# Kernel optimization log

Measured on AMD Instinct MI355X. Metric: run time of the kernel, lower is better.

Reference implementation:

```python
import jax, jax.numpy as jnp
import numpy as np

N, E, F, H, D, O = 100000, 1600000, 128, 128, 64, 1


def setup_inputs() -> dict:
    key = jax.random.key(0)
    ks = jax.random.split(key, 10)
    s = lambda f: np.float32(1.0 / np.sqrt(f))
    return {
        "x": jax.random.normal(ks[0], (N, F), jnp.float32),
        "edge_index": jax.random.randint(ks[1], (2, E), 0, N),
        "W1": jax.random.normal(ks[2], (F, H), jnp.float32) * s(F),
        "b1": jnp.zeros((H,), jnp.float32),
        "Wh": jax.random.normal(ks[3], (H, H), jnp.float32) * s(H),
        "bh": jnp.zeros((H,), jnp.float32),
        "W2": jax.random.normal(ks[4], (H, D), jnp.float32) * s(H),
        "b2": jnp.zeros((D,), jnp.float32),
        "Wo": jax.random.normal(ks[5], (D, O), jnp.float32) * s(D),
        "bo": jnp.zeros((O,), jnp.float32),
    }


def _gcn_layer(h, W, b, src, dst, norm, n):
    # linear transform then normalized sparse aggregation (GCNConv)
    h = h @ W                                   # [n, out]
    msg = h[src] * norm[:, None]                # gather + scale, [E+n, out]
    return jax.ops.segment_sum(msg, dst, num_segments=n) + b


def reference(x, edge_index, W1, b1, Wh, bh, W2, b2, Wo, bo):
    n = x.shape[0]
    loop = jnp.arange(n, dtype=edge_index.dtype)
    src = jnp.concatenate([edge_index[0], loop])  # add self loops
    dst = jnp.concatenate([edge_index[1], loop])
    deg = jax.ops.segment_sum(jnp.ones_like(dst, dtype=x.dtype), dst, num_segments=n)
    dinv = jnp.where(deg > 0, jax.lax.rsqrt(deg), 0.0)
    norm = dinv[src] * dinv[dst]                  # sym-normalized edge weights

    h = jax.nn.relu(_gcn_layer(x, W1, b1, src, dst, norm, n))
    h = jax.nn.relu(_gcn_layer(h, Wh, bh, src, dst, norm, n))
    z = _gcn_layer(h, W2, b2, src, dst, norm, n)  # embedding (no relu after gcn2)
    return z @ Wo + bo                            # node_classification logits [n, 1]
```

## Files before the change

kernel.cpp:

```cpp
#include <hip/hip_runtime.h>
#include <hip/hip_fp16.h>


#define CHUNK 8192
#define ASTR 136

using f16x8 = __attribute__((ext_vector_type(8))) _Float16;
using f32x4 = __attribute__((ext_vector_type(4))) float;

__global__ __launch_bounds__(256) void prep_w(const float* __restrict__ W1,
                                              const float* __restrict__ Wh,
                                              const float* __restrict__ W2,
                                              const float* __restrict__ b2,
                                              const float* __restrict__ Wo,
                                              const float* __restrict__ bo,
                                              __half* __restrict__ Wt1,
                                              __half* __restrict__ WtH,
                                              float* __restrict__ w3,
                                              float* __restrict__ c3) {
    const float* W = blockIdx.x ? Wh : W1;
    __half* Wt = blockIdx.x ? WtH : Wt1;
    for (int i = threadIdx.x; i < 16384; i += 256) {
        int c = i >> 7, k = i & 127;
        Wt[c * 128 + k] = __float2half(W[k * 128 + c]);
    }
    if (blockIdx.x == 0 && threadIdx.x < 128) {
        int j = threadIdx.x;
        float s = 0.f;
        for (int d = 0; d < 64; ++d) s += W2[j * 64 + d] * Wo[d];
        w3[j] = s;
        if (j == 0) {
            float c = 0.f;
            for (int d = 0; d < 64; ++d) c += b2[d] * Wo[d];
            *c3 = c + bo[0];
        }
    }
}

__device__ __forceinline__ void hist_body(const int* __restrict__ dst,
                                          int* __restrict__ hist,
                                          int E, int NBKT, int NB, int blk) {
    __shared__ int bins[1024];
    for (int i = threadIdx.x; i < NBKT; i += 256) bins[i] = 0;
    __syncthreads();
    int beg = blk * CHUNK, end = min(E, beg + CHUNK);
    for (int e = beg + threadIdx.x; e < end; e += 256)
        atomicAdd(&bins[dst[e] >> 7], 1);
    __syncthreads();
    for (int i = threadIdx.x; i < NBKT; i += 256)
        hist[i * NB + blk] = bins[i];
}

template<typename AT>
__device__ __forceinline__ void gemm_body(const AT* __restrict__ A,
                                          const __half* __restrict__ Wt,
                                          __half* __restrict__ Ch, int n, int blk) {
    __shared__ _Float16 Al[64 * ASTR];
    __shared__ _Float16 Wl[128 * ASTR];
    const int tid = threadIdx.x;
    const int row0 = blk * 64;

#pragma unroll
    for (int i = 0; i < 8; ++i) {
        int idx = tid + 256 * i;
        int c = idx >> 4, q = idx & 15;
        uint4 v = *(const uint4*)(Wt + c * 128 + q * 8);
        *(uint4*)(&Wl[c * ASTR + q * 8]) = v;
    }
#pragma unroll
    for (int i = 0; i < 4; ++i) {
        int idx = tid + 256 * i;
        int r = idx >> 4, q = idx & 15;
        int row = row0 + r;
        uint4 u;
        if constexpr (sizeof(AT) == 2) {
            u = (row < n) ? *(const uint4*)((const __half*)A + (size_t)row * 128 + q * 8)
                          : make_uint4(0u, 0u, 0u, 0u);
        } else {
            if (row < n) {
                const float* ap = (const float*)A + (size_t)row * 128 + q * 8;
                float4 v0 = *(const float4*)ap;
                float4 v1 = *(const float4*)(ap + 4);
                __half2 p0 = __floats2half2_rn(v0.x, v0.y);
                __half2 p1 = __floats2half2_rn(v0.z, v0.w);
                __half2 p2 = __floats2half2_rn(v1.x, v1.y);
                __half2 p3 = __floats2half2_rn(v1.z, v1.w);
                u.x = *(unsigned*)&p0; u.y = *(unsigned*)&p1;
                u.z = *(unsigned*)&p2; u.w = *(unsigned*)&p3;
            } else u = make_uint4(0u, 0u, 0u, 0u);
        }
        *(uint4*)(&Al[r * ASTR + q * 8]) = u;
    }
    __syncthreads();

    const int wave = tid >> 6, lane = tid & 63;
    const int wr = (wave >> 1) * 32;
    const int wc = (wave & 1) * 64;
    const int l = lane & 15, g = lane >> 4;

    f32x4 acc[2][4];
#pragma unroll
    for (int i = 0; i < 2; ++i)
#pragma unroll
        for (int j = 0; j < 4; ++j) acc[i][j] = (f32x4){0.f, 0.f, 0.f, 0.f};

#pragma unroll
    for (int kk = 0; kk < 128; kk += 32) {
        int ko = kk + g * 8;
        f16x8 a0 = *(const f16x8*)(&Al[(wr + l) * ASTR + ko]);
        f16x8 a1 = *(const f16x8*)(&Al[(wr + 16 + l) * ASTR + ko]);
        f16x8 b0 = *(const f16x8*)(&Wl[(wc + l) * ASTR + ko]);
        f16x8 b1 = *(const f16x8*)(&Wl[(wc + 16 + l) * ASTR + ko]);
        f16x8 b2 = *(const f16x8*)(&Wl[(wc + 32 + l) * ASTR + ko]);
        f16x8 b3 = *(const f16x8*)(&Wl[(wc + 48 + l) * ASTR + ko]);
        acc[0][0] = __builtin_amdgcn_mfma_f32_16x16x32_f16(a0, b0, acc[0][0], 0, 0, 0);
        acc[0][1] = __builtin_amdgcn_mfma_f32_16x16x32_f16(a0, b1, acc[0][1], 0, 0, 0);
        acc[0][2] = __builtin_amdgcn_mfma_f32_16x16x32_f16(a0, b2, acc[0][2], 0, 0, 0);
        acc[0][3] = __builtin_amdgcn_mfma_f32_16x16x32_f16(a0, b3, acc[0][3], 0, 0, 0);
        acc[1][0] = __builtin_amdgcn_mfma_f32_16x16x32_f16(a1, b0, acc[1][0], 0, 0, 0);
        acc[1][1] = __builtin_amdgcn_mfma_f32_16x16x32_f16(a1, b1, acc[1][1], 0, 0, 0);
        acc[1][2] = __builtin_amdgcn_mfma_f32_16x16x32_f16(a1, b2, acc[1][2], 0, 0, 0);
        acc[1][3] = __builtin_amdgcn_mfma_f32_16x16x32_f16(a1, b3, acc[1][3], 0, 0, 0);
    }

#pragma unroll
    for (int rt = 0; rt < 2; ++rt) {
#pragma unroll
        for (int j = 0; j < 4; ++j) {
            int row = row0 + wr + rt * 16 + g * 4 + j;
            if (row < n) {
#pragma unroll
                for (int ct = 0; ct < 4; ++ct)
                    Ch[(size_t)row * 128 + wc + ct * 16 + l] =
                        __float2half(acc[rt][ct][j]);
            }
        }
    }
}

__global__ __launch_bounds__(256) void mega1(const int* __restrict__ dst,
                                             int* __restrict__ hist,
                                             int E, int NBKT, int NB,
                                             const float* __restrict__ x,
                                             const __half* __restrict__ Wt1,
                                             __half* __restrict__ g1, int n) {
    if ((int)blockIdx.x < NB)
        hist_body(dst, hist, E, NBKT, NB, blockIdx.x);
    else
        gemm_body<float>(x, Wt1, g1, n, blockIdx.x - NB);
}

__global__ __launch_bounds__(256) void gemm2_k(const __half* __restrict__ A,
                                               const __half* __restrict__ Wt,
                                               __half* __restrict__ Ch, int n) {
    gemm_body<__half>(A, Wt, Ch, n, blockIdx.x);
}

__global__ __launch_bounds__(256) void scanA(int* __restrict__ hist, int* __restrict__ binsum,
                                             int NBKT, int NB) {
    int wave = (int)((blockIdx.x * (size_t)blockDim.x + threadIdx.x) >> 6);
    if (wave >= NBKT) return;
    int lane = threadIdx.x & 63;
    int* row = hist + (size_t)wave * NB;
    int running = 0;
    for (int b0 = 0; b0 < NB; b0 += 64) {
        int idx = b0 + lane;
        int v = (idx < NB) ? row[idx] : 0;
        int s = v;
#pragma unroll
        for (int off = 1; off < 64; off <<= 1) {
            int u = __shfl_up(s, off, 64);
            if (lane >= off) s += u;
        }
        if (idx < NB) row[idx] = running + s - v;
        running += __shfl(s, 63, 64);
    }
    if (lane == 0) binsum[wave] = running;
}

__global__ void scanK2(const int* __restrict__ binsum, int* __restrict__ binbase,
                       int NBKT, int E) {
    __shared__ int s[1024];
    int t = threadIdx.x;
    int v = (t < NBKT) ? binsum[t] : 0;
    s[t] = v;
    __syncthreads();
    for (int off = 1; off < 1024; off <<= 1) {
        int u = (t >= off) ? s[t - off] : 0;
        __syncthreads();
        s[t] += u;
        __syncthreads();
    }
    if (t < NBKT) binbase[t] = s[t] - v;
    if (t == 0) binbase[NBKT] = E;
}

__global__ __launch_bounds__(256) void scatterH(const int* __restrict__ src,
                                                const int* __restrict__ dst,
                                                const int* __restrict__ hist,
                                                const int* __restrict__ binbase,
                                                int* __restrict__ tmp,
                                                int E, int NBKT, int NB) {
    __shared__ int offs[1024];
    int blk = blockIdx.x;
    for (int i = threadIdx.x; i < NBKT; i += 256)
        offs[i] = hist[i * NB + blk] + binbase[i];
    __syncthreads();
    int beg = blk * CHUNK, end = min(E, beg + CHUNK);
    for (int e = beg + threadIdx.x; e < end; e += 256) {
        int d = dst[e];
        int pos = atomicAdd(&offs[d >> 7], 1);
        tmp[pos] = ((d & 127) << 17) | src[e];
    }
}

#define EBUF 2688
__global__ __launch_bounds__(256) void bucket_csr(const int* __restrict__ tmp,
                                                  const int* __restrict__ binbase,
                                                  int* __restrict__ rowptr,
                                                  int* __restrict__ srcidx,
                                                  float* __restrict__ dinv,
                                                  int n) {
    __shared__ int cnt[128], sc[128], cnt2[128];
    __shared__ int ebuf[EBUF];
    int b = blockIdx.x;
    int bstart = binbase[b], bend = binbase[b + 1];
    int cntE = bend - bstart;
    bool fit = (cntE <= EBUF);
    if (threadIdx.x < 128) cnt[threadIdx.x] = 0;
    __syncthreads();
    for (int e = threadIdx.x; e < cntE; e += 256) {
        int p = tmp[bstart + e];
        if (fit) ebuf[e] = p;
        atomicAdd(&cnt[p >> 17], 1);
    }
    __syncthreads();
    if (threadIdx.x < 128) sc[threadIdx.x] = cnt[threadIdx.x];
    __syncthreads();
    for (int off = 1; off < 128; off <<= 1) {
        int u = 0;
        if (threadIdx.x < 128 && threadIdx.x >= off) u = sc[threadIdx.x - off];
        __syncthreads();
        if (threadIdx.x < 128) sc[threadIdx.x] += u;
        __syncthreads();
    }
    if (threadIdx.x < 128) {
        int excl = sc[threadIdx.x] - cnt[threadIdx.x];
        cnt2[threadIdx.x] = excl;
        int id = b * 128 + threadIdx.x;
        if (id <= n) rowptr[id] = bstart + excl;
        if (id < n) dinv[id] = rsqrtf((float)cnt[threadIdx.x] + 1.0f);
    }
    __syncthreads();
    for (int e = threadIdx.x; e < cntE; e += 256) {
        int p = fit ? ebuf[e] : tmp[bstart + e];
        int pos = bstart + atomicAdd(&cnt2[p >> 17], 1);
        srcidx[pos] = p & 0x1FFFF;
    }
}

template<int MODE, int EDGE_DINV>
__global__ __launch_bounds__(256) void agg_csr(const int* __restrict__ rowptr,
                                               const int* __restrict__ srcidx,
                                               const float* __restrict__ dinv,
                                               const __half* __restrict__ Gh,
                                               const float* __restrict__ bias,
                                               const float* __restrict__ w3,
                                               void* __restrict__ outp, int n) {
    int node = (int)((blockIdx.x * (size_t)blockDim.x + threadIdx.x) >> 5);
    if (node >= n) return;
    const int lane = threadIdx.x & 63;
    const int l32 = lane & 31;
    const int strm = l32 >> 4;
    const int l = l32 & 15;
    const int co = l * 8;
    int beg = rowptr[node], end = rowptr[node + 1];
    float di = dinv[node];

    float4 aLo = make_float4(0.f, 0.f, 0.f, 0.f);
    float4 aHi = make_float4(0.f, 0.f, 0.f, 0.f);

#define ACCS(u, s)                                                          \
    {                                                                       \
        float2 f0 = __half22float2(*(const __half2*)&(u).x);                \
        float2 f1 = __half22float2(*(const __half2*)&(u).y);                \
        float2 f2 = __half22float2(*(const __half2*)&(u).z);                \
        float2 f3 = __half22float2(*(const __half2*)&(u).w);                \
        aLo.x = fmaf(f0.x, s, aLo.x); aLo.y = fmaf(f0.y, s, aLo.y);         \
        aLo.z = fmaf(f1.x, s, aLo.z); aLo.w = fmaf(f1.y, s, aLo.w);         \
        aHi.x = fmaf(f2.x, s, aHi.x); aHi.y = fmaf(f2.y, s, aHi.y);         \
        aHi.z = fmaf(f3.x, s, aHi.z); aHi.w = fmaf(f3.y, s, aHi.w);         \
    }

    if (strm == 0) {
        uint4 u = *(const uint4*)(Gh + (size_t)node * 128 + co);
        float sf = EDGE_DINV ? di : 1.0f;
        ACCS(u, sf);
    }

    int e = beg + strm;
    for (; e + 6 < end; e += 8) {
        int s0 = srcidx[e], s1 = srcidx[e + 2], s2 = srcidx[e + 4], s3 = srcidx[e + 6];
        float d0 = 1.f, d1 = 1.f, d2 = 1.f, d3 = 1.f;
        if (EDGE_DINV) { d0 = dinv[s0]; d1 = dinv[s1]; d2 = dinv[s2]; d3 = dinv[s3]; }
        uint4 u0 = *(const uint4*)(Gh + (size_t)s0 * 128 + co);
        uint4 u1 = *(const uint4*)(Gh + (size_t)s1 * 128 + co);
        uint4 u2 = *(const uint4*)(Gh + (size_t)s2 * 128 + co);
        uint4 u3 = *(const uint4*)(Gh + (size_t)s3 * 128 + co);
        ACCS(u0, d0);
        ACCS(u1, d1);
        ACCS(u2, d2);
        ACCS(u3, d3);
    }
    for (; e < end; e += 2) {
        int s0 = srcidx[e];
        float d0 = EDGE_DINV ? dinv[s0] : 1.0f;
        uint4 u0 = *(const uint4*)(Gh + (size_t)s0 * 128 + co);
        ACCS(u0, d0);
    }
#undef ACCS

    aLo.x += __shfl_xor(aLo.x, 16, 64); aLo.y += __shfl_xor(aLo.y, 16, 64);
    aLo.z += __shfl_xor(aLo.z, 16, 64); aLo.w += __shfl_xor(aLo.w, 16, 64);
    aHi.x += __shfl_xor(aHi.x, 16, 64); aHi.y += __shfl_xor(aHi.y, 16, 64);
    aHi.z += __shfl_xor(aHi.z, 16, 64); aHi.w += __shfl_xor(aHi.w, 16, 64);

    float4 b0 = *(const float4*)(bias + co);
    float4 b1 = *(const float4*)(bias + co + 4);
    float o0 = fmaxf(di * aLo.x + b0.x, 0.f);
    float o1 = fmaxf(di * aLo.y + b0.y, 0.f);
    float o2 = fmaxf(di * aLo.z + b0.z, 0.f);
    float o3 = fmaxf(di * aLo.w + b0.w, 0.f);
    float o4 = fmaxf(di * aHi.x + b1.x, 0.f);
    float o5 = fmaxf(di * aHi.y + b1.y, 0.f);
    float o6 = fmaxf(di * aHi.z + b1.z, 0.f);
    float o7 = fmaxf(di * aHi.w + b1.w, 0.f);

    if constexpr (MODE == 0) {
        if (strm == 0) {
            __half2 p0 = __floats2half2_rn(di * o0, di * o1);
            __half2 p1 = __floats2half2_rn(di * o2, di * o3);
            __half2 p2 = __floats2half2_rn(di * o4, di * o5);
            __half2 p3 = __floats2half2_rn(di * o6, di * o7);
            uint4 u;
            u.x = *(unsigned*)&p0; u.y = *(unsigned*)&p1;
            u.z = *(unsigned*)&p2; u.w = *(unsigned*)&p3;
            *(uint4*)((__half*)outp + (size_t)node * 128 + co) = u;
        }
    } else {
        float4 w0 = *(const float4*)(w3 + co);
        float4 w1 = *(const float4*)(w3 + co + 4);
        float v = o0 * w0.x + o1 * w0.y + o2 * w0.z + o3 * w0.w
                + o4 * w1.x + o5 * w1.y + o6 * w1.z + o7 * w1.w;
        v += __shfl_xor(v, 1, 64);
        v += __shfl_xor(v, 2, 64);
        v += __shfl_xor(v, 4, 64);
        v += __shfl_xor(v, 8, 64);
        if (l32 == 0) ((float*)outp)[node] = di * v;
    }
}

__global__ void agg_csr_scalar(const int* __restrict__ rowptr, const int* __restrict__ srcidx,
                               const float* __restrict__ dinv, const float* __restrict__ ys,
                               const float* __restrict__ c3, float* __restrict__ out, int n) {
    int i = blockIdx.x * blockDim.x + threadIdx.x;
    if (i >= n) return;
    int beg = rowptr[i], end = rowptr[i + 1];
    float acc = ys[i];
    int e = beg;
    for (; e + 3 < end; e += 4) {
        acc += ys[srcidx[e]] + ys[srcidx[e + 1]] + ys[srcidx[e + 2]] + ys[srcidx[e + 3]];
    }
    for (; e < end; ++e) acc += ys[srcidx[e]];
    out[i] = dinv[i] * acc + c3[0];
}

static inline size_t align4(size_t x) { return (x + 3) & ~(size_t)3; }

extern "C" void kernel_launch(void* const* d_in, const int* in_sizes, int n_in,
                              void* d_out, int out_size, void* d_ws, size_t ws_size,
                              hipStream_t stream) {
    const float* x  = (const float*)d_in[0];
    const int* ei   = (const int*)d_in[1];
    const float* W1 = (const float*)d_in[2];
    const float* b1 = (const float*)d_in[3];
    const float* Wh = (const float*)d_in[4];
    const float* bh = (const float*)d_in[5];
    const float* W2 = (const float*)d_in[6];
    const float* b2 = (const float*)d_in[7];
    const float* Wo = (const float*)d_in[8];
    const float* bo = (const float*)d_in[9];
    float* out = (float*)d_out;

    const int n = in_sizes[0] / 128;
    const int E = in_sizes[1] / 2;
    const int* src = ei;
    const int* dst = ei + E;

    const int NB = (E + CHUNK - 1) / CHUNK;
    const int NBKT = (n >> 7) + 1;

    size_t o = 0;
    int* rowptr = (int*)d_ws + o;        o = align4(o + n + 1);
    int* srcidx = (int*)d_ws + o;        o = align4(o + E);
    int* tmp    = (int*)d_ws + o;        o = align4(o + E);
    int* hist   = (int*)d_ws + o;        o = align4(o + (size_t)NBKT * NB);
    int* binsum = (int*)d_ws + o;        o = align4(o + NBKT);
    int* binbase= (int*)d_ws + o;        o = align4(o + NBKT + 1);
    float* dinv = (float*)d_ws + o;      o = align4(o + n);
    float* w3   = (float*)d_ws + o;      o = align4(o + 128);
    float* c3   = (float*)d_ws + o;      o = align4(o + 4);
    __half* Wt1 = (__half*)((int*)d_ws + o);     o = align4(o + 8192);
    __half* WtH = (__half*)((int*)d_ws + o);     o = align4(o + 8192);
    __half* bufA16 = (__half*)((int*)d_ws + o);  o = align4(o + (size_t)n * 64);
    __half* bufB16 = (__half*)((int*)d_ws + o);  o = align4(o + (size_t)n * 64);
    float* ys = (float*)bufB16;

    const int B = (n + 255) / 256;
    const int GG = (n + 63) / 64;
    const int GA = (int)(((size_t)n * 32 + 255) / 256);

    prep_w<<<2, 256, 0, stream>>>(W1, Wh, W2, b2, Wo, bo, Wt1, WtH, w3, c3);

    mega1<<<NB + GG, 256, 0, stream>>>(dst, hist, E, NBKT, NB, x, Wt1, bufA16, n);

    scanA<<<(NBKT * 64 + 255) / 256, 256, 0, stream>>>(hist, binsum, NBKT, NB);
    scanK2<<<1, 1024, 0, stream>>>(binsum, binbase, NBKT, E);
    scatterH<<<NB, 256, 0, stream>>>(src, dst, hist, binbase, tmp, E, NBKT, NB);
    bucket_csr<<<NBKT, 256, 0, stream>>>(tmp, binbase, rowptr, srcidx, dinv, n);

    agg_csr<0, 1><<<GA, 256, 0, stream>>>(rowptr, srcidx, dinv, bufA16, b1, w3, bufB16, n);

    gemm2_k<<<GG, 256, 0, stream>>>(bufB16, WtH, bufA16, n);
    agg_csr<1, 0><<<GA, 256, 0, stream>>>(rowptr, srcidx, dinv, bufA16, bh, w3, ys, n);

    agg_csr_scalar<<<B, 256, 0, stream>>>(rowptr, srcidx, dinv, ys, c3, out, n);
}
```

Baseline: 222.4 us.

## Regroup kernel launches: fuse weight prep with histogram, scatter with first GEMM

Weight transpose and conversion now runs as two extra blocks of the histogram kernel, removing the separate prep_w launch. The first-layer GEMM moves out of that kernel into a combined launch with the edge scatter, so the GEMM runs concurrently with scattering instead of with histogramming. The intent is to save one launch and let the scatter work overlap the GEMM. As a side effect the histogram kernel runs alone, with only two small prep blocks alongside it.

```diff
diff --git a/kernel.cpp b/kernel.cpp
--- a/kernel.cpp
+++ b/kernel.cpp
@@ -8,23 +8,38 @@
 using f16x8 = __attribute__((ext_vector_type(8))) _Float16;
 using f32x4 = __attribute__((ext_vector_type(4))) float;
 
-__global__ __launch_bounds__(256) void prep_w(const float* __restrict__ W1,
-                                              const float* __restrict__ Wh,
-                                              const float* __restrict__ W2,
-                                              const float* __restrict__ b2,
-                                              const float* __restrict__ Wo,
-                                              const float* __restrict__ bo,
-                                              __half* __restrict__ Wt1,
-                                              __half* __restrict__ WtH,
-                                              float* __restrict__ w3,
-                                              float* __restrict__ c3) {
-    const float* W = blockIdx.x ? Wh : W1;
-    __half* Wt = blockIdx.x ? WtH : Wt1;
+__device__ __forceinline__ void hist_body(const int* __restrict__ dst,
+                                          int* __restrict__ hist,
+                                          int E, int NBKT, int NB, int blk) {
+    __shared__ int bins[1024];
+    for (int i = threadIdx.x; i < NBKT; i += 256) bins[i] = 0;
+    __syncthreads();
+    int beg = blk * CHUNK, end = min(E, beg + CHUNK);
+    for (int e = beg + threadIdx.x; e < end; e += 256)
+        atomicAdd(&bins[dst[e] >> 7], 1);
+    __syncthreads();
+    for (int i = threadIdx.x; i < NBKT; i += 256)
+        hist[i * NB + blk] = bins[i];
+}
+
+__device__ __forceinline__ void prep_body(int which,
+                                          const float* __restrict__ W1,
+                                          const float* __restrict__ Wh,
+                                          const float* __restrict__ W2,
+                                          const float* __restrict__ b2,
+                                          const float* __restrict__ Wo,
+                                          const float* __restrict__ bo,
+                                          __half* __restrict__ Wt1,
+                                          __half* __restrict__ WtH,
+                                          float* __restrict__ w3,
+                                          float* __restrict__ c3) {
+    const float* W = which ? Wh : W1;
+    __half* Wt = which ? WtH : Wt1;
     for (int i = threadIdx.x; i < 16384; i += 256) {
         int c = i >> 7, k = i & 127;
         Wt[c * 128 + k] = __float2half(W[k * 128 + c]);
     }
-    if (blockIdx.x == 0 && threadIdx.x < 128) {
+    if (which == 0 && threadIdx.x < 128) {
         int j = threadIdx.x;
         float s = 0.f;
         for (int d = 0; d < 64; ++d) s += W2[j * 64 + d] * Wo[d];
@@ -37,18 +52,22 @@
     }
 }
 
-__device__ __forceinline__ void hist_body(const int* __restrict__ dst,
-                                          int* __restrict__ hist,
-                                          int E, int NBKT, int NB, int blk) {
-    __shared__ int bins[1024];
-    for (int i = threadIdx.x; i < NBKT; i += 256) bins[i] = 0;
+__device__ __forceinline__ void scatter_body(const int* __restrict__ src,
+                                             const int* __restrict__ dst,
+                                             const int* __restrict__ hist,
+                                             const int* __restrict__ binbase,
+                                             int* __restrict__ tmp,
+                                             int E, int NBKT, int NB, int blk) {
+    __shared__ int offs[1024];
+    for (int i = threadIdx.x; i < NBKT; i += 256)
+        offs[i] = hist[i * NB + blk] + binbase[i];
     __syncthreads();
     int beg = blk * CHUNK, end = min(E, beg + CHUNK);
-    for (int e = beg + threadIdx.x; e < end; e += 256)
-        atomicAdd(&bins[dst[e] >> 7], 1);
-    __syncthreads();
-    for (int i = threadIdx.x; i < NBKT; i += 256)
-        hist[i * NB + blk] = bins[i];
+    for (int e = beg + threadIdx.x; e < end; e += 256) {
+        int d = dst[e];
+        int pos = atomicAdd(&offs[d >> 7], 1);
+        tmp[pos] = ((d & 127) << 17) | src[e];
+    }
 }
 
 template<typename AT>
@@ -141,11 +160,33 @@
 __global__ __launch_bounds__(256) void mega1(const int* __restrict__ dst,
                                              int* __restrict__ hist,
                                              int E, int NBKT, int NB,
+                                             const float* __restrict__ W1,
+                                             const float* __restrict__ Wh,
+                                             const float* __restrict__ W2,
+                                             const float* __restrict__ b2,
+                                             const float* __restrict__ Wo,
+                                             const float* __restrict__ bo,
+                                             __half* __restrict__ Wt1,
+                                             __half* __restrict__ WtH,
+                                             float* __restrict__ w3,
+                                             float* __restrict__ c3) {
+    if ((int)blockIdx.x < NB)
+        hist_body(dst, hist, E, NBKT, NB, blockIdx.x);
+    else
+        prep_body(blockIdx.x - NB, W1, Wh, W2, b2, Wo, bo, Wt1, WtH, w3, c3);
+}
+
+__global__ __launch_bounds__(256) void mega3(const int* __restrict__ src,
+                                             const int* __restrict__ dst,
+                                             const int* __restrict__ hist,
+                                             const int* __restrict__ binbase,
+                                             int* __restrict__ tmp,
+                                             int E, int NBKT, int NB,
                                              const float* __restrict__ x,
                                              const __half* __restrict__ Wt1,
                                              __half* __restrict__ g1, int n) {
     if ((int)blockIdx.x < NB)
-        hist_body(dst, hist, E, NBKT, NB, blockIdx.x);
+        scatter_body(src, dst, hist, binbase, tmp, E, NBKT, NB, blockIdx.x);
     else
         gemm_body<float>(x, Wt1, g1, n, blockIdx.x - NB);
 }
@@ -193,25 +234,6 @@
     }
     if (t < NBKT) binbase[t] = s[t] - v;
     if (t == 0) binbase[NBKT] = E;
-}
-
-__global__ __launch_bounds__(256) void scatterH(const int* __restrict__ src,
-                                                const int* __restrict__ dst,
-                                                const int* __restrict__ hist,
-                                                const int* __restrict__ binbase,
-                                                int* __restrict__ tmp,
-                                                int E, int NBKT, int NB) {
-    __shared__ int offs[1024];
-    int blk = blockIdx.x;
-    for (int i = threadIdx.x; i < NBKT; i += 256)
-        offs[i] = hist[i * NB + blk] + binbase[i];
-    __syncthreads();
-    int beg = blk * CHUNK, end = min(E, beg + CHUNK);
-    for (int e = beg + threadIdx.x; e < end; e += 256) {
-        int d = dst[e];
-        int pos = atomicAdd(&offs[d >> 7], 1);
-        tmp[pos] = ((d & 127) << 17) | src[e];
-    }
 }
 
 #define EBUF 2688
@@ -420,19 +442,15 @@
     const int GG = (n + 63) / 64;
     const int GA = (int)(((size_t)n * 32 + 255) / 256);
 
-    prep_w<<<2, 256, 0, stream>>>(W1, Wh, W2, b2, Wo, bo, Wt1, WtH, w3, c3);
-
-    mega1<<<NB + GG, 256, 0, stream>>>(dst, hist, E, NBKT, NB, x, Wt1, bufA16, n);
-
+    mega1<<<NB + 2, 256, 0, stream>>>(dst, hist, E, NBKT, NB,
+                                      W1, Wh, W2, b2, Wo, bo, Wt1, WtH, w3, c3);
     scanA<<<(NBKT * 64 + 255) / 256, 256, 0, stream>>>(hist, binsum, NBKT, NB);
     scanK2<<<1, 1024, 0, stream>>>(binsum, binbase, NBKT, E);
-    scatterH<<<NB, 256, 0, stream>>>(src, dst, hist, binbase, tmp, E, NBKT, NB);
+    mega3<<<NB + GG, 256, 0, stream>>>(src, dst, hist, binbase, tmp, E, NBKT, NB,
+                                       x, Wt1, bufA16, n);
     bucket_csr<<<NBKT, 256, 0, stream>>>(tmp, binbase, rowptr, srcidx, dinv, n);
-
     agg_csr<0, 1><<<GA, 256, 0, stream>>>(rowptr, srcidx, dinv, bufA16, b1, w3, bufB16, n);
-
     gemm2_k<<<GG, 256, 0, stream>>>(bufB16, WtH, bufA16, n);
     agg_csr<1, 0><<<GA, 256, 0, stream>>>(rowptr, srcidx, dinv, bufA16, bh, w3, ys, n);
-
     agg_csr_scalar<<<B, 256, 0, stream>>>(rowptr, srcidx, dinv, ys, c3, out, n);
 }
```

Measured after the change: 208.4 us. -6.3%, faster.
